# Kernel optimization log

Measured on AMD Instinct MI355X. Metric: run time of the kernel, lower is better.

The kernel has to match this reference:

```python
import jax, jax.numpy as jnp
import numpy as np

D_MODEL = 1024
NUM_HEADS = 16
DEPTH = D_MODEL // NUM_HEADS


def setup_inputs() -> dict:
    key = jax.random.key(0)
    ks = jax.random.split(key, 12)
    B, S = 4, 2048
    scale = 1.0 / np.sqrt(D_MODEL)
    inp = {
        "query": jax.random.normal(ks[0], (B, S, D_MODEL), jnp.float32),
        "key": jax.random.normal(ks[1], (B, S, D_MODEL), jnp.float32),
        "value": jax.random.normal(ks[2], (B, S, D_MODEL), jnp.float32),
        "mask": jnp.zeros((B, 1, 1, S), jnp.float32),  # 1.0 => masked position
        "wq": jax.random.normal(ks[3], (D_MODEL, D_MODEL), jnp.float32) * scale,
        "bq": jnp.zeros((D_MODEL,), jnp.float32),
        "wk": jax.random.normal(ks[4], (D_MODEL, D_MODEL), jnp.float32) * scale,
        "bk": jnp.zeros((D_MODEL,), jnp.float32),
        "wv": jax.random.normal(ks[5], (D_MODEL, D_MODEL), jnp.float32) * scale,
        "bv": jnp.zeros((D_MODEL,), jnp.float32),
        "wo": jax.random.normal(ks[6], (D_MODEL, D_MODEL), jnp.float32) * scale,
        "bo": jnp.zeros((D_MODEL,), jnp.float32),
    }
    return inp


def _split_heads(x, B):
    # (B, S, d_model) -> (B, H, S, depth)
    return x.reshape(B, -1, NUM_HEADS, DEPTH).transpose(0, 2, 1, 3)


def reference(query, key, value, mask, wq, bq, wk, bk, wv, bv, wo, bo):
    B, Sq, _ = query.shape
    q = _split_heads(query @ wq + bq, B)   # (B,H,Sq,dh)
    k = _split_heads(key @ wk + bk, B)     # (B,H,Sk,dh)
    v = _split_heads(value @ wv + bv, B)   # (B,H,Sk,dh)

    logits = jnp.einsum("bhqd,bhkd->bhqk", q, k) / jnp.sqrt(
        jnp.asarray(DEPTH, q.dtype))
    logits = logits + mask * (-1e9)
    attn = jax.nn.softmax(logits, axis=-1)
    ctx = jnp.einsum("bhqk,bhkd->bhqd", attn, v)
    ctx = ctx.transpose(0, 2, 1, 3).reshape(B, Sq, D_MODEL)
    return ctx @ wo + bo
```

## Files before the change

### kernel.cpp

```cpp
#include <hip/hip_runtime.h>
#include <stdint.h>


typedef unsigned short u16;
typedef __attribute__((ext_vector_type(8))) short bf16x8;
typedef __attribute__((ext_vector_type(4))) short bf16x4;
typedef __attribute__((ext_vector_type(4))) float f32x4;

#define LOG2E 1.4426950408889634f

__device__ __forceinline__ u16 f2bf(float f) {
  uint32_t u = __builtin_bit_cast(uint32_t, f);
  u += 0x7fffu + ((u >> 16) & 1u);
  return (u16)(u >> 16);
}
__device__ __forceinline__ uint32_t cvt_pk(float a, float b) {
  uint32_t r;
  asm("v_cvt_pk_bf16_f32 %0, %1, %2" : "=v"(r) : "v"(a), "v"(b));
  return r;
}
__device__ __forceinline__ void gload16(const u16* g, u16* l) {
  __builtin_amdgcn_global_load_lds(
      (const __attribute__((address_space(1))) uint32_t*)(const void*)g,
      (__attribute__((address_space(3))) uint32_t*)(void*)l, 16, 0, 0);
}
__device__ __forceinline__ f32x4 mfma16(bf16x4 a, bf16x4 b, f32x4 c) {
#if __has_builtin(__builtin_amdgcn_mfma_f32_16x16x16bf16_1k)
  return __builtin_amdgcn_mfma_f32_16x16x16bf16_1k(a, b, c, 0, 0, 0);
#else
  f32x4 d = c;
  asm volatile("v_mfma_f32_16x16x16_bf16 %0, %1, %2, %0"
               : "+v"(d) : "v"(a), "v"(b));
  return d;
#endif
}

__global__ __launch_bounds__(256) void convert_x(
    const float* __restrict__ X, u16* __restrict__ Xb)
{
  const size_t i = ((size_t)blockIdx.x * 256 + threadIdx.x) * 8;
  const float4 a = *(const float4*)(X + i);
  const float4 b = *(const float4*)(X + i + 4);
  uint4 o;
  o.x = cvt_pk(a.x, a.y); o.y = cvt_pk(a.z, a.w);
  o.z = cvt_pk(b.x, b.y); o.w = cvt_pk(b.z, b.w);
  *(uint4*)(Xb + i) = o;
}

__global__ __launch_bounds__(256) void prep_mask(
    const float* __restrict__ mask, float* __restrict__ M2)
{
  const int i = blockIdx.x * 256 + threadIdx.x;
  M2[i] = mask[i] * (-1.0e9f * LOG2E);
}

__global__ __launch_bounds__(256) void transpose_w(
    const float* __restrict__ W0, const float* __restrict__ W1,
    const float* __restrict__ W2, const float* __restrict__ W3,
    u16* __restrict__ Wt)
{
  const int z = blockIdx.z;
  const float* W = (z == 0) ? W0 : (z == 1) ? W1 : (z == 2) ? W2 : W3;
  u16* T = Wt + ((size_t)z << 20);
  const int n0 = blockIdx.x * 64, k0 = blockIdx.y * 64;
  const int tid = threadIdx.x;
  const int r = tid >> 4, c4 = (tid & 15) * 4;
  __shared__ float t[64][65];
#pragma unroll
  for (int j = 0; j < 4; ++j) {
    const int row = r + j * 16;
    const float4 v = *(const float4*)(W + (size_t)(k0 + row) * 1024 + n0 + c4);
    t[c4 + 0][row] = v.x; t[c4 + 1][row] = v.y;
    t[c4 + 2][row] = v.z; t[c4 + 3][row] = v.w;
  }
  __syncthreads();
#pragma unroll
  for (int j = 0; j < 4; ++j) {
    const int nrow = r + j * 16;
    uint2 o;
    o.x = cvt_pk(t[nrow][c4 + 0], t[nrow][c4 + 1]);
    o.y = cvt_pk(t[nrow][c4 + 2], t[nrow][c4 + 3]);
    *(uint2*)(T + (size_t)(n0 + nrow) * 1024 + k0 + c4) = o;
  }
}

__global__ __launch_bounds__(256) void gemm_proj(
    const u16* __restrict__ A, const u16* __restrict__ Wt,
    const float* __restrict__ Bi, u16* __restrict__ O16,
    float* __restrict__ O32, int mode)
{
  const int bid = blockIdx.x;
  const int nid = (bid & 7) * 64 + (bid >> 3);
  const int n0 = (nid & 7) * 128;
  const int m0 = (nid >> 3) * 128;
  const int tid = threadIdx.x;
  const int w = tid >> 6, l = tid & 63, lo = l & 15, hi = l >> 4;
  const int wr = w >> 1, wc = w & 1;

  __shared__ __align__(16) u16 As[128 * 32];
  __shared__ __align__(16) u16 Bs[128 * 32];

  const f32x4 fz = {0.f, 0.f, 0.f, 0.f};
  f32x4 acc[4][4];
#pragma unroll
  for (int m = 0; m < 4; ++m)
#pragma unroll
    for (int n = 0; n < 4; ++n) acc[m][n] = fz;

  const int srow = w * 32 + (l >> 2);
  const u16* ga = A  + (size_t)(m0 + srow) * 1024 + (l & 3) * 8;
  const u16* gb = Wt + (size_t)(n0 + srow) * 1024 + (l & 3) * 8;
  u16* lA0 = &As[w * 1024];  u16* lA1 = &As[w * 1024 + 512];
  u16* lB0 = &Bs[w * 1024];  u16* lB1 = &Bs[w * 1024 + 512];

  for (int k0 = 0; k0 < 1024; k0 += 32) {
    __syncthreads();
    gload16(ga,             lA0);
    gload16(ga + 16 * 1024, lA1);
    gload16(gb,             lB0);
    gload16(gb + 16 * 1024, lB1);
    ga += 32; gb += 32;
    __syncthreads();

    bf16x8 af[4], bf[4];
#pragma unroll
    for (int m = 0; m < 4; ++m)
      af[m] = *(const bf16x8*)&As[(wr * 64 + m * 16 + lo) * 32 + hi * 8];
#pragma unroll
    for (int n = 0; n < 4; ++n)
      bf[n] = *(const bf16x8*)&Bs[(wc * 64 + n * 16 + lo) * 32 + hi * 8];
#pragma unroll
    for (int m = 0; m < 4; ++m)
#pragma unroll
      for (int n = 0; n < 4; ++n)
        acc[m][n] = __builtin_amdgcn_mfma_f32_16x16x32_bf16(af[m], bf[n], acc[m][n], 0, 0, 0);
  }

#pragma unroll
  for (int m = 0; m < 4; ++m) {
#pragma unroll
    for (int n = 0; n < 4; ++n) {
      const int col = n0 + wc * 64 + n * 16 + lo;
      const float bc = Bi[col];
      const int h = col >> 6, d = col & 63;
#pragma unroll
      for (int i = 0; i < 4; ++i) {
        const int r = m0 + wr * 64 + m * 16 + hi * 4 + i;
        const int b = r >> 11, s = r & 2047;
        float v = acc[m][n][i] + bc;
        if (mode == 0) {
          v *= 0.125f * LOG2E;
          O16[((size_t)((b * 16 + h) * 2048 + s)) * 64 + d] = f2bf(v);
        } else if (mode == 1) {
          O16[((size_t)((b * 16 + h) * 2048 + s)) * 64 + d] = f2bf(v);
        } else if (mode == 2) {
          O16[((size_t)((b * 16 + h) * 64 + d)) * 2048 + s] = f2bf(v);
        } else {
          O32[(size_t)r * 1024 + col] = v;
        }
      }
    }
  }
}

__global__ __launch_bounds__(512, 4) void attn(
    const u16* __restrict__ Q, const u16* __restrict__ K,
    const u16* __restrict__ Vt, const float* __restrict__ M2,
    u16* __restrict__ Ctx)
{
  const int bid = blockIdx.x;
  const int nid = (bid & 7) * 64 + (bid >> 3);
  const int qt = nid & 7;
  const int bh = nid >> 3;
  const int b = bh >> 4, h = bh & 15;
  const int tid = threadIdx.x;
  const int w = tid >> 6, l = tid & 63, lo = l & 15, hi = l >> 4;

  __shared__ __align__(16) u16 Kl[2][4096];
  __shared__ __align__(16) u16 Vl[2][4096];
  __shared__ __align__(16) float Msk[2048];

  const u16* Qb = Q + (size_t)bh * (2048 * 64);
  const u16* Kb = K + (size_t)bh * (2048 * 64);
  const u16* Vb = Vt + (size_t)bh * (64 * 2048);

  *(float4*)&Msk[tid * 4] = *(const float4*)(M2 + (size_t)b * 2048 + tid * 4);

  const int qrow0 = qt * 256 + w * 32 + lo;
  const bf16x8 qa00 = *(const bf16x8*)(Qb + (size_t)qrow0 * 64 + hi * 8);
  const bf16x8 qa01 = *(const bf16x8*)(Qb + (size_t)qrow0 * 64 + 32 + hi * 8);
  const bf16x8 qa10 = *(const bf16x8*)(Qb + (size_t)(qrow0 + 16) * 64 + hi * 8);
  const bf16x8 qa11 = *(const bf16x8*)(Qb + (size_t)(qrow0 + 16) * 64 + 32 + hi * 8);

  const f32x4 fz = {0.f, 0.f, 0.f, 0.f};
  f32x4 o0[4] = {fz, fz, fz, fz};
  f32x4 o1[4] = {fz, fz, fz, fz};
  f32x4 ol0 = fz, ol1 = fz;
  const short oneb = (short)0x3F80;
  const bf16x4 ones = {oneb, oneb, oneb, oneb};
  const int lo7 = lo & 7;

  const int rowA = tid >> 3;
  const int slA  = (tid & 7) ^ (rowA & 7);
  const u16* gK = Kb + (size_t)rowA * 64 + slA * 8;
  const u16* gV = Vb + (size_t)rowA * 2048 + slA * 8;

#define STAGE(kt_, buf_)                                    \
  do {                                                      \
    gload16(gK + (size_t)(kt_) * 4096, &Kl[buf_][w * 512]); \
    gload16(gV + (kt_) * 64,           &Vl[buf_][w * 512]); \
  } while (0)

  STAGE(0, 0);
  __syncthreads();

  for (int kt = 0; kt < 32; ++kt) {
    const int cur = kt & 1;
    STAGE((kt + 1) & 31, cur ^ 1);
    asm volatile("s_waitcnt vmcnt(2)" ::: "memory");
    __builtin_amdgcn_s_barrier();

    const int kv0 = kt * 64;
    const u16* Kc = &Kl[cur][0];
    const u16* Vc = &Vl[cur][0];

    f32x4 st0[4], st1[4];
    __builtin_amdgcn_s_setprio(1);
#pragma unroll
    for (int f = 0; f < 4; ++f) {
      const int krow = (f * 16 + lo) * 64;
      const bf16x8 kb0 = *(const bf16x8*)&Kc[krow + ((hi ^ lo7) << 3)];
      const bf16x8 kb1 = *(const bf16x8*)&Kc[krow + (((4 + hi) ^ lo7) << 3)];
      const f32x4 c = *(const f32x4*)&Msk[kv0 + 16 * f + 4 * hi];
      f32x4 a0 = __builtin_amdgcn_mfma_f32_16x16x32_bf16(kb0, qa00, c, 0, 0, 0);
      st0[f] = __builtin_amdgcn_mfma_f32_16x16x32_bf16(kb1, qa01, a0, 0, 0, 0);
      f32x4 a1 = __builtin_amdgcn_mfma_f32_16x16x32_bf16(kb0, qa10, c, 0, 0, 0);
      st1[f] = __builtin_amdgcn_mfma_f32_16x16x32_bf16(kb1, qa11, a1, 0, 0, 0);
    }
    __builtin_amdgcn_s_setprio(0);

    union { uint32_t u[2]; bf16x4 v; } pa0[4], pa1[4];
#pragma unroll
    for (int f = 0; f < 4; ++f) {
      pa0[f].u[0] = cvt_pk(exp2f(st0[f][0]), exp2f(st0[f][1]));
      pa0[f].u[1] = cvt_pk(exp2f(st0[f][2]), exp2f(st0[f][3]));
      pa1[f].u[0] = cvt_pk(exp2f(st1[f][0]), exp2f(st1[f][1]));
      pa1[f].u[1] = cvt_pk(exp2f(st1[f][2]), exp2f(st1[f][3]));
    }

    __builtin_amdgcn_s_setprio(1);
#pragma unroll
    for (int f = 0; f < 4; ++f) {
      ol0 = mfma16(pa0[f].v, ones, ol0);
      ol1 = mfma16(pa1[f].v, ones, ol1);
#pragma unroll
      for (int nf = 0; nf < 4; ++nf) {
        const int vrow = (lo + 16 * nf) * 64;
        const int slot = (((2 * f + (hi >> 1)) ^ lo7) << 3) + ((hi & 1) << 2);
        const bf16x4 vb = *(const bf16x4*)&Vc[vrow + slot];
        o0[nf] = mfma16(pa0[f].v, vb, o0[nf]);
        o1[nf] = mfma16(pa1[f].v, vb, o1[nf]);
      }
    }
    __builtin_amdgcn_s_setprio(0);

    asm volatile("s_waitcnt lgkmcnt(0)" ::: "memory");
    __builtin_amdgcn_s_barrier();
  }
#undef STAGE

  float inv0[4], inv1[4];
#pragma unroll
  for (int i = 0; i < 4; ++i) { inv0[i] = 1.f / ol0[i]; inv1[i] = 1.f / ol1[i]; }
#pragma unroll
  for (int nf = 0; nf < 4; ++nf) {
#pragma unroll
    for (int i = 0; i < 4; ++i) {
      const int s0 = qt * 256 + w * 32 + hi * 4 + i;
      const int d = nf * 16 + lo;
      Ctx[((size_t)((b * 2048 + s0) * 16 + h)) * 64 + d] = f2bf(o0[nf][i] * inv0[i]);
      Ctx[((size_t)((b * 2048 + s0 + 16) * 16 + h)) * 64 + d] = f2bf(o1[nf][i] * inv1[i]);
    }
  }
}

extern "C" void kernel_launch(void* const* d_in, const int* in_sizes, int n_in,
                              void* d_out, int out_size, void* d_ws, size_t ws_size,
                              hipStream_t stream) {
  const float* q_in = (const float*)d_in[0];
  const float* k_in = (const float*)d_in[1];
  const float* v_in = (const float*)d_in[2];
  const float* mask = (const float*)d_in[3];
  const float* wq = (const float*)d_in[4];
  const float* bq = (const float*)d_in[5];
  const float* wk = (const float*)d_in[6];
  const float* bk = (const float*)d_in[7];
  const float* wv = (const float*)d_in[8];
  const float* bv = (const float*)d_in[9];
  const float* wo = (const float*)d_in[10];
  const float* bo = (const float*)d_in[11];

  u16* ws  = (u16*)d_ws;
  u16* wtq = ws;
  u16* wtk = wtq + (1u << 20);
  u16* wtv = wtk + (1u << 20);
  u16* wto = wtv + (1u << 20);
  u16* Qb  = wto + (1u << 20);
  u16* Kb  = Qb + (size_t)8192 * 1024;
  u16* Vtb = Kb + (size_t)8192 * 1024;
  u16* xbf = Vtb + (size_t)8192 * 1024;
  u16* ctx = xbf;
  float* M2 = (float*)(xbf + (size_t)8192 * 1024);

  transpose_w<<<dim3(16, 16, 4), 256, 0, stream>>>(wq, wk, wv, wo, wtq);
  prep_mask<<<32, 256, 0, stream>>>(mask, M2);

  convert_x<<<4096, 256, 0, stream>>>(q_in, xbf);
  gemm_proj<<<512, 256, 0, stream>>>(xbf, wtq, bq, Qb, nullptr, 0);
  convert_x<<<4096, 256, 0, stream>>>(k_in, xbf);
  gemm_proj<<<512, 256, 0, stream>>>(xbf, wtk, bk, Kb, nullptr, 1);
  convert_x<<<4096, 256, 0, stream>>>(v_in, xbf);
  gemm_proj<<<512, 256, 0, stream>>>(xbf, wtv, bv, Vtb, nullptr, 2);

  attn<<<512, 512, 0, stream>>>(Qb, Kb, Vtb, M2, ctx);

  gemm_proj<<<512, 256, 0, stream>>>(ctx, wto, bo, nullptr, (float*)d_out, 3);
}
```

Measured before the change: 264.5 us.

## Double-buffer LDS tiles in projection GEMM to overlap loads with MFMA

Splits the shared-memory A/B tiles into two buffers and prefetches the next K-slice via global_load_lds while the current slice is consumed by MFMAs. Synchronization uses explicit vmcnt/lgkmcnt waits with raw s_barrier instead of __syncthreads. Aims to hide global load latency behind compute, at the cost of doubled LDS usage and a redundant wrap-around prefetch on the last iteration.

```diff
diff --git a/kernel.cpp b/kernel.cpp
--- a/kernel.cpp
+++ b/kernel.cpp
@@ -97,8 +97,8 @@
   const int w = tid >> 6, l = tid & 63, lo = l & 15, hi = l >> 4;
   const int wr = w >> 1, wc = w & 1;
 
-  __shared__ __align__(16) u16 As[128 * 32];
-  __shared__ __align__(16) u16 Bs[128 * 32];
+  __shared__ __align__(16) u16 As[2][4096];
+  __shared__ __align__(16) u16 Bs[2][4096];
 
   const f32x4 fz = {0.f, 0.f, 0.f, 0.f};
   f32x4 acc[4][4];
@@ -110,31 +110,41 @@
   const int srow = w * 32 + (l >> 2);
   const u16* ga = A  + (size_t)(m0 + srow) * 1024 + (l & 3) * 8;
   const u16* gb = Wt + (size_t)(n0 + srow) * 1024 + (l & 3) * 8;
-  u16* lA0 = &As[w * 1024];  u16* lA1 = &As[w * 1024 + 512];
-  u16* lB0 = &Bs[w * 1024];  u16* lB1 = &Bs[w * 1024 + 512];
-
-  for (int k0 = 0; k0 < 1024; k0 += 32) {
-    __syncthreads();
-    gload16(ga,             lA0);
-    gload16(ga + 16 * 1024, lA1);
-    gload16(gb,             lB0);
-    gload16(gb + 16 * 1024, lB1);
-    ga += 32; gb += 32;
-    __syncthreads();
+
+#define GST(k0_, b_)                                        \
+  do {                                                      \
+    gload16(ga + (k0_),             &As[b_][w * 1024]);     \
+    gload16(ga + (k0_) + 16 * 1024, &As[b_][w * 1024 + 512]); \
+    gload16(gb + (k0_),             &Bs[b_][w * 1024]);     \
+    gload16(gb + (k0_) + 16 * 1024, &Bs[b_][w * 1024 + 512]); \
+  } while (0)
+
+  GST(0, 0);
+  __syncthreads();
+
+  for (int kt = 0; kt < 32; ++kt) {
+    const int cur = kt & 1;
+    GST(((kt + 1) & 31) * 32, cur ^ 1);
+    asm volatile("s_waitcnt vmcnt(4)" ::: "memory");
+    __builtin_amdgcn_s_barrier();
 
     bf16x8 af[4], bf[4];
 #pragma unroll
     for (int m = 0; m < 4; ++m)
-      af[m] = *(const bf16x8*)&As[(wr * 64 + m * 16 + lo) * 32 + hi * 8];
+      af[m] = *(const bf16x8*)&As[cur][(wr * 64 + m * 16 + lo) * 32 + hi * 8];
 #pragma unroll
     for (int n = 0; n < 4; ++n)
-      bf[n] = *(const bf16x8*)&Bs[(wc * 64 + n * 16 + lo) * 32 + hi * 8];
+      bf[n] = *(const bf16x8*)&Bs[cur][(wc * 64 + n * 16 + lo) * 32 + hi * 8];
 #pragma unroll
     for (int m = 0; m < 4; ++m)
 #pragma unroll
       for (int n = 0; n < 4; ++n)
         acc[m][n] = __builtin_amdgcn_mfma_f32_16x16x32_bf16(af[m], bf[n], acc[m][n], 0, 0, 0);
-  }
+
+    asm volatile("s_waitcnt lgkmcnt(0)" ::: "memory");
+    __builtin_amdgcn_s_barrier();
+  }
+#undef GST
 
 #pragma unroll
   for (int m = 0; m < 4; ++m) {
```

Result: no change. 264.9 us (+0.2%).
